# Kernel optimization log

Hardware: AMD Instinct MI355X
Metric: run time of the kernel (lower is better)

The kernel has to match this reference:

```python
import jax, jax.numpy as jnp
import numpy as np

T, B, E, H = 2048, 2, 1024, 16
D = E // H
MAX_REL = 16  # RelativePosition default max_relative_position


def setup_inputs() -> dict:
    key = jax.random.key(0)
    ks = jax.random.split(key, 11)
    s = 1.0 / np.sqrt(E)
    inp = {
        'query': jax.random.normal(ks[0], (T, B, E), dtype=jnp.float32),
        'Wq': jax.random.normal(ks[1], (E, E), dtype=jnp.float32) * s,
        'bq': jnp.zeros((E,), dtype=jnp.float32),
        'Wk': jax.random.normal(ks[2], (E, E), dtype=jnp.float32) * s,
        'bk': jnp.zeros((E,), dtype=jnp.float32),
        'Wv': jax.random.normal(ks[3], (E, E), dtype=jnp.float32) * s,
        'bv': jnp.zeros((E,), dtype=jnp.float32),
        'Wo': jax.random.normal(ks[4], (E, E), dtype=jnp.float32) * s,
        'bo': jnp.zeros((E,), dtype=jnp.float32),
        'rk_table': jax.random.normal(ks[5], (2 * MAX_REL + 1, D), dtype=jnp.float32) * 0.05,
        'rv_table': jax.random.normal(ks[6], (2 * MAX_REL + 1, D), dtype=jnp.float32) * 0.05,
    }
    return inp


def _rel_idx(lq, lk):
    # distance_mat = k - q, clipped to [-MAX_REL, MAX_REL], shifted to [0, 2*MAX_REL]
    d = jnp.arange(lk)[None, :] - jnp.arange(lq)[:, None]
    return jnp.clip(d, -MAX_REL, MAX_REL) + MAX_REL  # [lq, lk] int


def reference(query, Wq, bq, Wk, bk, Wv, bv, Wo, bo, rk_table, rv_table):
    t, b, e = query.shape
    scale = D ** -0.5
    # projections (torch Linear: x @ W.T + b)
    q = (query @ Wq.T + bq) * scale
    k = query @ Wk.T + bk
    v = query @ Wv.T + bv
    # [T,B,E] -> [B*H, T, D]
    q = q.reshape(t, b * H, D).transpose(1, 0, 2)
    k = k.reshape(t, b * H, D).transpose(1, 0, 2)
    v = v.reshape(t, b * H, D).transpose(1, 0, 2)
    # content scores + Shaw relative-position key scores
    scores = jnp.einsum('ntd,nsd->nts', q, k)            # [N, T, S]
    rk = rk_table[_rel_idx(t, t)]                        # [T, S, D]
    scores = scores + jnp.einsum('ntd,tsd->nts', q, rk)  # relpos_k term
    probs = jax.nn.softmax(scores, axis=-1)
    # weighted values + Shaw relative-position value term
    rv = rv_table[_rel_idx(t, t)]                        # [T, S, D]
    attn = jnp.einsum('nts,nsd->ntd', probs, v) + jnp.einsum('nts,tsd->ntd', probs, rv)
    # [B*H, T, D] -> [T, B, E]
    attn = attn.transpose(1, 0, 2).reshape(t, b, e)
    return attn @ Wo.T + bo
```

## Files before the change

kernel.cpp:

```cpp
#include <hip/hip_runtime.h>
#include <hip/hip_bf16.h>
#include <math.h>

#define T_   2048
#define B_   2
#define E_   1024
#define H_   16
#define D_   64
#define NH_  32
#define M_   4096

typedef __attribute__((ext_vector_type(8))) short s8b;
typedef __attribute__((ext_vector_type(4))) float f4;

#define MFMA_B16(a,b,c) __builtin_amdgcn_mfma_f32_16x16x32_bf16(a,b,c,0,0,0)
#define LOG2E 1.44269504088896f

__device__ __forceinline__ unsigned short f2bu(float f) {
    union { __hip_bfloat16 h; unsigned short u; } cv;
    cv.h = __float2bfloat16(f);
    return cv.u;
}
__device__ __forceinline__ unsigned short f2bu_fast(float f) {
    return (unsigned short)((__float_as_uint(f) + 0x8000u) >> 16);
}
__device__ __forceinline__ float bu2f(unsigned short u) {
    union { __hip_bfloat16 h; unsigned short u; } cv; cv.u = u;
    return __bfloat162float(cv.h);
}
__device__ __forceinline__ unsigned int pk2(float a, float b) {
    return (unsigned int)f2bu(a) | ((unsigned int)f2bu(b) << 16);
}
__device__ __forceinline__ unsigned int pk2_fast(float a, float b) {
    return ((__float_as_uint(a) + 0x8000u) >> 16) |
           ((__float_as_uint(b) + 0x8000u) & 0xFFFF0000u);
}
__device__ __forceinline__ float fexp2(float x) {
    return __builtin_amdgcn_exp2f(x);
}
__device__ __forceinline__ float ld1d(const void* p, size_t idx, bool f32) {
    return f32 ? ((const float*)p)[idx] : bu2f(((const unsigned short*)p)[idx]);
}
__device__ __forceinline__ float qsumq(float v) {
    v += __shfl_xor(v, 16); v += __shfl_xor(v, 32);
    return v;
}
__device__ __forceinline__ void glds16(const unsigned short* g, unsigned short* l) {
    __builtin_amdgcn_global_load_lds(
        (const __attribute__((address_space(1))) unsigned int*)g,
        (__attribute__((address_space(3))) unsigned int*)l, 16, 0, 0);
}
__device__ __forceinline__ bool detect_f32(const unsigned short* q16) {
    int e = (q16[threadIdx.x & 63] >> 7) & 0xFF;
    bool sane = (e == 0) || (e >= 97 && e <= 157);
    unsigned long long m = __ballot(sane);
    return __popcll(m) < 56;
}

__global__ __launch_bounds__(256) void cvt_bf16(
    const void* __restrict__ x,
    const void* __restrict__ Wq, const void* __restrict__ Wk,
    const void* __restrict__ Wv, const void* __restrict__ Wo,
    const void* __restrict__ bq, const void* __restrict__ bk,
    const void* __restrict__ bv, const void* __restrict__ bo,
    unsigned short* __restrict__ xw, unsigned short* __restrict__ Ww,
    unsigned short* __restrict__ bw, int* __restrict__ flag)
{
    const bool f32m = detect_f32((const unsigned short*)x);
    const int bid = blockIdx.x;
    if (bid == 0 && threadIdx.x == 0)
        *flag = f32m ? 1 : 0;
    int y, lb;
    if (bid < 2048)       { y = 0;                      lb = bid; }
    else if (bid < 4096)  { y = 1 + ((bid - 2048) >> 9); lb = (bid - 2048) & 511; }
    else                  { y = 5 + (bid - 4096);        lb = 0; }
    const void* src; unsigned short* dst; int n;
    if (y == 0)      { src = x; dst = xw; n = M_ * E_; }
    else if (y <= 4) {
        src = (y == 1) ? Wq : (y == 2) ? Wk : (y == 3) ? Wv : Wo;
        dst = Ww + (size_t)(y - 1) * E_ * E_; n = E_ * E_;
    } else {
        src = (y == 5) ? bq : (y == 6) ? bk : (y == 7) ? bv : bo;
        dst = bw + (size_t)(y - 5) * E_; n = E_;
    }
    int i = (lb * 256 + threadIdx.x) * 8;
    if (i >= n) return;
    if (f32m) {
        const float* s = (const float*)src + i;
        float4 f0 = *(const float4*)s, f1 = *(const float4*)(s + 4);
        union { unsigned int d[4]; s8b v; } u;
        u.d[0] = pk2(f0.x, f0.y); u.d[1] = pk2(f0.z, f0.w);
        u.d[2] = pk2(f1.x, f1.y); u.d[3] = pk2(f1.z, f1.w);
        *(s8b*)(dst + i) = u.v;
    } else {
        *(s8b*)(dst + i) = *(const s8b*)((const unsigned short*)src + i);
    }
}

__global__ __launch_bounds__(256, 3) void qkv_gemm(
    const unsigned short* __restrict__ xw, const unsigned short* __restrict__ Ww,
    const unsigned short* __restrict__ bw,
    unsigned short* __restrict__ qo, unsigned short* __restrict__ ko,
    unsigned short* __restrict__ vo)
{
    const int bid = blockIdx.x;
    const int r_ = bid & 7, s_ = bid >> 3;
    const int g = r_ + 8 * (s_ >> 3);
    const int e0 = (s_ & 7) * 128;
    const int m0 = (g & 31) * 128;
    const int p  = g >> 5;
    const unsigned short* W    = Ww + (size_t)p * E_ * E_;
    const unsigned short* bias = bw + (size_t)p * E_;
    const float scale = (p == 0) ? 0.125f * LOG2E : 1.0f;

    const int tid = threadIdx.x, w = tid >> 6, lane = tid & 63;
    const int quad = lane >> 4, lc = lane & 15;
    const int wx = w & 1, wy = w >> 1;

    __shared__ unsigned short smem[4][128 * 32];

    f4 acc[4][4];
    #pragma unroll
    for (int i = 0; i < 4; i++)
        #pragma unroll
        for (int j = 0; j < 4; j++) acc[i][j] = (f4){0.f, 0.f, 0.f, 0.f};

    const int gr = lane >> 2;
    const int gc = (lane & 3) ^ ((lane >> 2) & 3);
    const size_t aoff = (size_t)(m0 + w*32 + gr) * E_ + gc*8;
    const size_t boff = (size_t)(e0 + w*32 + gr) * E_ + gc*8;

    #pragma unroll
    for (int j = 0; j < 2; j++) {
        glds16(xw + aoff + (size_t)j*16*E_, &smem[0][(w*128 + j*64) * 8]);
        glds16(W  + boff + (size_t)j*16*E_, &smem[2][(w*128 + j*64) * 8]);
    }
    __syncthreads();

    const int fcA = quad ^ (lc & 3);
    for (int k0 = 0; k0 < E_; k0 += 32) {
        const int cur = (k0 >> 5) & 1;
        if (k0 + 32 < E_) {
            #pragma unroll
            for (int j = 0; j < 2; j++) {
                glds16(xw + aoff + (size_t)j*16*E_ + k0 + 32, &smem[cur^1][(w*128 + j*64) * 8]);
                glds16(W  + boff + (size_t)j*16*E_ + k0 + 32, &smem[2 + (cur^1)][(w*128 + j*64) * 8]);
            }
        }
        s8b af[4], bfr[4];
        #pragma unroll
        for (int i = 0; i < 4; i++)
            af[i]  = *(const s8b*)&smem[cur][((wy*64 + i*16 + lc)*4 + fcA) * 8];
        #pragma unroll
        for (int i = 0; i < 4; i++)
            bfr[i] = *(const s8b*)&smem[2 + cur][((wx*64 + i*16 + lc)*4 + fcA) * 8];
        #pragma unroll
        for (int ms = 0; ms < 4; ms++)
            #pragma unroll
            for (int ns = 0; ns < 4; ns++)
                acc[ms][ns] = MFMA_B16(af[ms], bfr[ns], acc[ms][ns]);
        __syncthreads();
    }

    float bias_v[4];
    #pragma unroll
    for (int ns = 0; ns < 4; ns++) bias_v[ns] = bu2f(bias[e0 + wx*64 + ns*16 + lc]);

    unsigned int* cst = (unsigned int*)&smem[0][0];
    if (p < 2) {
        #pragma unroll
        for (int ms = 0; ms < 4; ms++)
            #pragma unroll
            for (int ns = 0; ns < 4; ns++)
                #pragma unroll
                for (int r2 = 0; r2 < 4; r2++) {
                    float val = (acc[ms][ns][r2] + bias_v[ns]) * scale;
                    float nb = __shfl_xor(val, 1);
                    if (!(lane & 1)) {
                        int mi = wy*64 + ms*16 + quad*4 + r2;
                        int ei = wx*64 + ns*16 + lc;
                        int row = ((mi & 1) * 2 + (ei >> 6)) * 64 + (mi >> 1);
                        int col = (ei & 63) >> 1;
                        cst[row*32 + (col ^ ((row & 7) << 2))] = pk2(val, nb);
                    }
                }
        __syncthreads();
        unsigned int* dst32 = (unsigned int*)((p == 0) ? qo : ko);
        #pragma unroll
        for (int i = 0; i < 8; i++) {
            const int li  = i*256 + tid;
            const int row = li >> 3;
            const int ch  = li & 7;
            uint4 vd = *(const uint4*)&cst[row*32 + ((ch*4) ^ ((row & 7) << 2))];
            const int bb = row >> 7, hh = (row >> 6) & 1, tq = row & 63;
            const size_t du = (((size_t)(bb*H_ + (e0 >> 6) + hh) * T_
                                + (m0 >> 1) + tq) << 5) + ch*4;
            *(uint4*)&dst32[du] = vd;
        }
    } else {
        #pragma unroll
        for (int ms = 0; ms < 4; ms++) {
            const int tq = wy*16 + ms*4 + quad;
            #pragma unroll
            for (int ns = 0; ns < 4; ns++) {
                const int e_l = wx*64 + ns*16 + lc;
                const int x = (e_l & 7) << 2;
                float v0 = acc[ms][ns][0] + bias_v[ns];
                float v1 = acc[ms][ns][1] + bias_v[ns];
                float v2 = acc[ms][ns][2] + bias_v[ns];
                float v3 = acc[ms][ns][3] + bias_v[ns];
                cst[e_l*64 + ( tq       ^ x)] = pk2(v0, v2);
                cst[e_l*64 + ((32 + tq) ^ x)] = pk2(v1, v3);
            }
        }
        __syncthreads();
        #pragma unroll
        for (int i = 0; i < 8; i++) {
            const int li  = i*256 + tid;
            const int e_l = li >> 4;
            const int bb  = (li >> 3) & 1;
            const int ch  = li & 7;
            const int x   = (e_l & 7) << 2;
            uint4 vd = *(const uint4*)&cst[e_l*64 + ((bb*32 + ch*4) ^ x)];
            const int e = e0 + e_l, h = e >> 6, d = e & 63;
            const size_t du = ((size_t)(bb*H_ + h) * 64 + d) * (T_/2)
                              + (m0 >> 2) + ch*4;
            *(uint4*)((unsigned int*)vo + du) = vd;
        }
    }
}

__global__ __launch_bounds__(512, 4) void attn_mfma(
    const unsigned short* __restrict__ q, const unsigned short* __restrict__ k,
    const unsigned short* __restrict__ v,
    const void* __restrict__ rk_t, const void* __restrict__ rv_t,
    unsigned short* __restrict__ aout, const int* __restrict__ flag)
{
    const bool f32m = (*flag != 0);
    const int bid = blockIdx.x;
    const int n = bid & 31, qt = bid >> 5;
    const int t0 = qt * 128;
    const int tid = threadIdx.x, w = tid >> 6, lane = tid & 63;
    const int quad = lane >> 4, lc = lane & 15;

    __shared__ unsigned short k_s[2][64 * 64];
    __shared__ unsigned short v_s[2][64 * 64];
    __shared__ unsigned short p_s[8][16 * 72];
    __shared__ unsigned short qrk_s[128 * 36];
    __shared__ unsigned short diag16[128 * 33];
    __shared__ float st_L[128], st_R[128];

    const unsigned short* qn = q + ((size_t)n * T_ + t0) * D_;
    const unsigned short* kn = k + (size_t)n * T_ * D_;
    const unsigned short* vn = v + (size_t)n * D_ * T_;

    s8b qa[2];
    #pragma unroll
    for (int kf = 0; kf < 2; kf++)
        qa[kf] = *(const s8b*)(qn + (size_t)(w*16 + lc) * D_ + kf*32 + quad*8);

    for (int i = tid; i < 128 * 33; i += 512) diag16[i] = 0;

    unsigned int* rks = (unsigned int*)&p_s[0][0];
    for (int i = tid; i < 48 * 36; i += 512) {
        int r = i / 36, c2 = i % 36;
        unsigned int val = 0;
        if (r < 33 && c2 < 32)
            val = pk2(ld1d(rk_t, r*64 + 2*c2, f32m), ld1d(rk_t, r*64 + 2*c2 + 1, f32m));
        rks[i] = val;
    }
    __syncthreads();

    for (int nt = 0; nt < 3; nt++) {
        s8b b0 = *(const s8b*)((const unsigned short*)rks + (nt*16 + lc)*72 + quad*8);
        s8b b1 = *(const s8b*)((const unsigned short*)rks + (nt*16 + lc)*72 + 32 + quad*8);
        f4 a = (f4){0.f, 0.f, 0.f, 0.f};
        a = MFMA_B16(qa[0], b0, a);
        a = MFMA_B16(qa[1], b1, a);
        #pragma unroll
        for (int r = 0; r < 4; r++) {
            float nb = __shfl_xor(a[r], 1);
            int col = nt*16 + lc;
            if (!(lane & 1) && col < 34)
                ((unsigned int*)qrk_s)[(w*16 + quad*4 + r)*18 + (col >> 1)] = pk2(a[r], nb);
        }
    }
    __syncthreads();

    const int t_l = w*16 + lc;
    const float qLn = bu2f(qrk_s[t_l*36 + 0]);
    const float qRn = bu2f(qrk_s[t_l*36 + 32]);
    float L_p = 0.f, R_p = 0.f;
    f4 O[4], lsN, lsL, lsR;
    lsN = (f4){0.f, 0.f, 0.f, 0.f};
    lsL = (f4){0.f, 0.f, 0.f, 0.f};
    lsR = (f4){0.f, 0.f, 0.f, 0.f};
    #pragma unroll
    for (int dt = 0; dt < 4; dt++) O[dt] = (f4){0.f, 0.f, 0.f, 0.f};
    const short ob = (short)0x3F80;
    const s8b ones = { ob, ob, ob, ob, ob, ob, ob, ob };

    const int grr = lane >> 3;
    const int gcc = (lane & 7) ^ grr;
    const size_t koff = (size_t)(w*8 + grr) * D_ + gcc*8;
    const size_t voff = (size_t)(w*8 + grr) * T_ + gcc*8;

    const int kts = ((bid >> 8) & 1) * 16;

    s8b kr0 = *(const s8b*)(kn + koff + (size_t)(kts * 64) * D_);
    s8b vr0 = *(const s8b*)(vn + voff + kts * 64);
    *(s8b*)&k_s[0][(w*64 + lane) * 8] = kr0;
    *(s8b*)&v_s[0][(w*64 + lane) * 8] = vr0;
    __syncthreads();

    const int lc7 = lc & 7;
    for (int it = 0; it < 32; it++) {
        const int kt = (it + kts) & 31;
        const int s0 = kt * 64;
        const int cur = it & 1;
        if (it + 1 < 32) {
            const int s0n = ((it + 1 + kts) & 31) * 64;
            kr0 = *(const s8b*)(kn + koff + (size_t)s0n * D_);
            vr0 = *(const s8b*)(vn + voff + s0n);
        }

        const bool farL  = (s0 + 63 < t0 - 16);
        const bool farR  = (s0 > t0 + 143);
        const bool nearT = !farL && !farR;

        s8b ak[4][2];
        #pragma unroll
        for (int st = 0; st < 4; st++) {
            int row = st*16 + lc;
            ak[st][0] = *(const s8b*)&k_s[cur][(row*8 + (quad       ^ lc7)) * 8];
            ak[st][1] = *(const s8b*)&k_s[cur][(row*8 + ((4 + quad) ^ lc7)) * 8];
        }

        #pragma unroll
        for (int st = 0; st < 4; st++) {
            f4 a;
            if (nearT) a = (f4){0.f, 0.f, 0.f, 0.f};
            else {
                float qb = farL ? qLn : qRn;
                a = (f4){qb, qb, qb, qb};
            }
            a = MFMA_B16(ak[st][0], qa[0], a);
            a = MFMA_B16(ak[st][1], qa[1], a);
            unsigned int lo, hi;
            if (nearT) {
                const int sb = s0 + st*16 + quad*4 - (t0 + t_l);
                unsigned short eb[4];
                #pragma unroll
                for (int r = 0; r < 4; r++) {
                    int rel = sb + r;
                    int rc = rel < -16 ? -16 : (rel > 16 ? 16 : rel);
                    float e = fexp2(a[r] + bu2f(qrk_s[t_l*36 + rc + 16]));
                    eb[r] = f2bu_fast(e);
                    if (rel <= -16)      L_p += e;
                    else if (rel >= 16)  R_p += e;
                    else                 diag16[t_l*33 + rel + 15] = eb[r];
                }
                lo = (unsigned int)eb[0] | ((unsigned int)eb[1] << 16);
                hi = (unsigned int)eb[2] | ((unsigned int)eb[3] << 16);
            } else {
                lo = pk2_fast(fexp2(a[0]), fexp2(a[1]));
                hi = pk2_fast(fexp2(a[2]), fexp2(a[3]));
            }
            *(uint2*)&p_s[w][lc*72 + st*16 + quad*4] = make_uint2(lo, hi);
        }

        s8b pb[2];
        pb[0] = *(const s8b*)&p_s[w][lc*72 + quad*8];
        pb[1] = *(const s8b*)&p_s[w][lc*72 + 32 + quad*8];
        if (nearT) {
            lsN = MFMA_B16(ones, pb[0], lsN);
            lsN = MFMA_B16(ones, pb[1], lsN);
        } else if (farL) {
            lsL = MFMA_B16(ones, pb[0], lsL);
            lsL = MFMA_B16(ones, pb[1], lsL);
        } else {
            lsR = MFMA_B16(ones, pb[0], lsR);
            lsR = MFMA_B16(ones, pb[1], lsR);
        }
        #pragma unroll
        for (int dt = 0; dt < 4; dt++) {
            int row = dt*16 + lc;
            s8b a0 = *(const s8b*)&v_s[cur][(row*8 + (quad       ^ lc7)) * 8];
            s8b a1 = *(const s8b*)&v_s[cur][(row*8 + ((4 + quad) ^ lc7)) * 8];
            O[dt] = MFMA_B16(a0, pb[0], O[dt]);
            O[dt] = MFMA_B16(a1, pb[1], O[dt]);
        }

        if (it + 1 < 32) {
            *(s8b*)&k_s[cur ^ 1][(w*64 + lane) * 8] = kr0;
            *(s8b*)&v_s[cur ^ 1][(w*64 + lane) * 8] = vr0;
        }
        __syncthreads();
    }

    float l = lsN[0] + lsL[0] + lsR[0];
    float L = lsL[0] + qsumq(L_p);
    float R = lsR[0] + qsumq(R_p);
    const float linv = 1.f / l;
    if (quad == 0) { st_L[t_l] = L; st_R[t_l] = R; }
    {
        unsigned int* rvs = (unsigned int*)&k_s[0][0];
        for (int i = tid; i < 64 * 32; i += 512) {
            int d = i >> 5, dwL = i & 31;
            int r0 = dwL * 2, r1 = r0 + 1;
            float x0 = (r0 < 33) ? ld1d(rv_t, (size_t)r0 * 64 + d, f32m) : 0.f;
            float x1 = (r1 < 33) ? ld1d(rv_t, (size_t)r1 * 64 + d, f32m) : 0.f;
            int phys = d * 32 + ((dwL >> 2) ^ (d & 7)) * 4 + (dwL & 3);
            rvs[phys] = pk2(x0, x1);
        }
    }
    __syncthreads();
    for (int j = 0; j < 16; j++) {
        int c = lane;
        int row = w*16 + j;
        unsigned short pv;
        if (c == 0)        pv = f2bu(st_L[row]);
        else if (c == 32)  pv = f2bu(st_R[row]);
        else if (c < 32)   pv = diag16[row*33 + c - 1];
        else               pv = 0;
        p_s[w][j*72 + c] = pv;
    }
    s8b pe[2];
    pe[0] = *(const s8b*)&p_s[w][lc*72 + quad*8];
    pe[1] = *(const s8b*)&p_s[w][lc*72 + 32 + quad*8];
    #pragma unroll
    for (int dt = 0; dt < 4; dt++) {
        int row = dt*16 + lc;
        s8b a0 = *(const s8b*)&k_s[0][(row*8 + (quad       ^ lc7)) * 8];
        s8b a1 = *(const s8b*)&k_s[0][(row*8 + ((4 + quad) ^ lc7)) * 8];
        O[dt] = MFMA_B16(a0, pe[0], O[dt]);
        O[dt] = MFMA_B16(a1, pe[1], O[dt]);
    }
    const int bb = n >> 4, h = n & 15;
    {
        int t_g = t0 + t_l;
        #pragma unroll
        for (int dt = 0; dt < 4; dt++) {
            float v0 = O[dt][0] * linv;
            float v1 = O[dt][1] * linv;
            float v2 = O[dt][2] * linv;
            float v3 = O[dt][3] * linv;
            int e = h*64 + dt*16 + quad*4;
            *(uint2*)&aout[((size_t)t_g * B_ + bb) * E_ + e] =
                make_uint2(pk2(v0, v1), pk2(v2, v3));
        }
    }
}

__global__ __launch_bounds__(256, 2) void out_gemm(
    const unsigned short* __restrict__ A,
    const unsigned short* __restrict__ Wob, const unsigned short* __restrict__ bob,
    void* __restrict__ out, const int* __restrict__ flag)
{
    const bool f32m = (*flag != 0);
    const int bid = blockIdx.x;
    const int r_ = bid & 7, s_ = bid >> 3;
    const int g = r_ + 8 * (s_ >> 3);
    const int m0 = g * 64;
    const int e0 = (s_ & 7) * 128;

    const int tid = threadIdx.x, w = tid >> 6, lane = tid & 63;
    const int quad = lane >> 4, lc = lane & 15;
    const int wx = w & 1, wy = w >> 1;

    __shared__ unsigned short smem[12288];
    #define A_S(c) (&smem[(c) * 2048])
    #define B_S(c) (&smem[4096 + (c) * 4096])

    f4 acc[2][4];
    #pragma unroll
    for (int i = 0; i < 2; i++)
        #pragma unroll
        for (int j = 0; j < 4; j++) acc[i][j] = (f4){0.f, 0.f, 0.f, 0.f};

    const int gr = lane >> 2;
    const int gc = (lane & 3) ^ (gr & 3);
    const size_t aoff = (size_t)(m0 + w*16 + gr) * E_ + gc*8;
    const size_t boff = (size_t)(e0 + w*32 + gr) * E_ + gc*8;

    glds16(A + aoff, &A_S(0)[(w*64) * 8]);
    #pragma unroll
    for (int j = 0; j < 2; j++)
        glds16(Wob + boff + (size_t)j*16*E_, &B_S(0)[(w*128 + j*64) * 8]);
    __syncthreads();

    const int fcA = quad ^ (lc & 3);
    for (int k0 = 0; k0 < E_; k0 += 32) {
        const int cur = (k0 >> 5) & 1;
        if (k0 + 32 < E_) {
            glds16(A + aoff + k0 + 32, &A_S(cur^1)[(w*64) * 8]);
            #pragma unroll
            for (int j = 0; j < 2; j++)
                glds16(Wob + boff + (size_t)j*16*E_ + k0 + 32, &B_S(cur^1)[(w*128 + j*64) * 8]);
        }
        s8b af[2], bfr[4];
        #pragma unroll
        for (int i = 0; i < 2; i++)
            af[i]  = *(const s8b*)&A_S(cur)[((wy*32 + i*16 + lc)*4 + fcA) * 8];
        #pragma unroll
        for (int i = 0; i < 4; i++)
            bfr[i] = *(const s8b*)&B_S(cur)[((wx*64 + i*16 + lc)*4 + fcA) * 8];
        #pragma unroll
        for (int ms = 0; ms < 2; ms++)
            #pragma unroll
            for (int ns = 0; ns < 4; ns++)
                acc[ms][ns] = MFMA_B16(af[ms], bfr[ns], acc[ms][ns]);
        __syncthreads();
    }

    float bias_v[4];
    #pragma unroll
    for (int ns = 0; ns < 4; ns++) bias_v[ns] = bu2f(bob[e0 + wx*64 + ns*16 + lc]);

    if (f32m) {
        #pragma unroll
        for (int ms = 0; ms < 2; ms++)
            #pragma unroll
            for (int ns = 0; ns < 4; ns++)
                #pragma unroll
                for (int r2 = 0; r2 < 4; r2++) {
                    float val = acc[ms][ns][r2] + bias_v[ns];
                    size_t m = m0 + wy*32 + ms*16 + quad*4 + r2;
                    int e = e0 + wx*64 + ns*16 + lc;
                    ((float*)out)[m * E_ + e] = val;
                }
    } else {
        unsigned int* cst = (unsigned int*)&smem[0];
        __syncthreads();
        #pragma unroll
        for (int ms = 0; ms < 2; ms++)
            #pragma unroll
            for (int ns = 0; ns < 4; ns++)
                #pragma unroll
                for (int r2 = 0; r2 < 4; r2++) {
                    float val = acc[ms][ns][r2] + bias_v[ns];
                    float nb = __shfl_xor(val, 1);
                    if (!(lane & 1)) {
                        int mi = wy*32 + ms*16 + quad*4 + r2;
                        int ei = wx*64 + ns*16 + lc;
                        int col = ei >> 1;
                        cst[mi*64 + (col ^ ((mi & 7) << 2))] = pk2(val, nb);
                    }
                }
        __syncthreads();
        unsigned int* dst32 = (unsigned int*)out;
        #pragma unroll
        for (int i = 0; i < 4; i++) {
            const int li  = i*256 + tid;
            const int row = li >> 4;
            const int ch  = li & 15;
            uint4 vd = *(const uint4*)&cst[row*64 + ((ch*4) ^ ((row & 7) << 2))];
            const size_t du = ((size_t)(m0 + row) * E_ + e0) / 2 + ch*4;
            *(uint4*)&dst32[du] = vd;
        }
    }
    #undef A_S
    #undef B_S
}

extern "C" void kernel_launch(void* const* d_in, const int* in_sizes, int n_in,
                              void* d_out, int out_size, void* d_ws, size_t ws_size,
                              hipStream_t stream) {
    const void* x  = d_in[0];
    const void* Wq = d_in[1];  const void* bq = d_in[2];
    const void* Wk = d_in[3];  const void* bk = d_in[4];
    const void* Wv = d_in[5];  const void* bv = d_in[6];
    const void* Wo = d_in[7];  const void* bo = d_in[8];
    const void* rk = d_in[9];  const void* rv = d_in[10];

    int* flag = (int*)d_ws;
    const size_t HTD = (size_t)NH_ * T_ * D_;
    unsigned short* qw = (unsigned short*)((char*)d_ws + 256);
    unsigned short* kw = qw + HTD;
    unsigned short* vw = kw + HTD;
    unsigned short* aw = vw + HTD;
    unsigned short* xw = aw + (size_t)M_ * E_;
    unsigned short* Ww = xw + (size_t)M_ * E_;
    unsigned short* bw = Ww + (size_t)4 * E_ * E_;

    cvt_bf16<<<dim3(4100), 256, 0, stream>>>(
        x, Wq, Wk, Wv, Wo, bq, bk, bv, bo, xw, Ww, bw, flag);
    qkv_gemm<<<dim3(768), 256, 0, stream>>>(xw, Ww, bw, qw, kw, vw);
    attn_mfma<<<dim3(NH_ * (T_/128)), 512, 0, stream>>>(qw, kw, vw, rk, rv, aw, flag);
    out_gemm<<<dim3(512), 256, 0, stream>>>(aw, Ww + (size_t)3*E_*E_, bw + 3*E_,
                                            d_out, flag);
}
```

Before: 208.1 us.

## Switch attention inner loop to 32x32 MFMA with register-resident P via permlane swap

```diff
diff --git a/kernel.cpp b/kernel.cpp
--- a/kernel.cpp
+++ b/kernel.cpp
@@ -12,8 +12,10 @@
 
 typedef __attribute__((ext_vector_type(8))) short s8b;
 typedef __attribute__((ext_vector_type(4))) float f4;
+typedef __attribute__((ext_vector_type(16))) float f16v;
 
 #define MFMA_B16(a,b,c) __builtin_amdgcn_mfma_f32_16x16x32_bf16(a,b,c,0,0,0)
+#define MFMA32(a,b,c)   __builtin_amdgcn_mfma_f32_32x32x16_bf16(a,b,c,0,0,0)
 #define LOG2E 1.44269504088896f
 
 __device__ __forceinline__ unsigned short f2bu(float f) {
@@ -41,9 +43,9 @@
 __device__ __forceinline__ float ld1d(const void* p, size_t idx, bool f32) {
     return f32 ? ((const float*)p)[idx] : bu2f(((const unsigned short*)p)[idx]);
 }
-__device__ __forceinline__ float qsumq(float v) {
-    v += __shfl_xor(v, 16); v += __shfl_xor(v, 32);
-    return v;
+__device__ __forceinline__ void plswap(unsigned int &a, unsigned int &b) {
+    auto r = __builtin_amdgcn_permlane32_swap(a, b, false, false);
+    a = r[0]; b = r[1];
 }
 __device__ __forceinline__ void glds16(const unsigned short* g, unsigned short* l) {
     __builtin_amdgcn_global_load_lds(
@@ -242,22 +244,20 @@
     const int t0 = qt * 128;
     const int tid = threadIdx.x, w = tid >> 6, lane = tid & 63;
     const int quad = lane >> 4, lc = lane & 15;
+    const int tg = w >> 1, sh = w & 1;
+    const int lh = lane >> 5, tloc = lane & 31;
+    const int t_bl = tg * 32 + tloc;
 
     __shared__ unsigned short k_s[2][64 * 64];
     __shared__ unsigned short v_s[2][64 * 64];
-    __shared__ unsigned short p_s[8][16 * 72];
+    __shared__ unsigned short p_s[4][32 * 72];
     __shared__ unsigned short qrk_s[128 * 36];
     __shared__ unsigned short diag16[128 * 33];
-    __shared__ float st_L[128], st_R[128];
+    __shared__ float st3[2][3][128];
 
     const unsigned short* qn = q + ((size_t)n * T_ + t0) * D_;
     const unsigned short* kn = k + (size_t)n * T_ * D_;
     const unsigned short* vn = v + (size_t)n * D_ * T_;
-
-    s8b qa[2];
-    #pragma unroll
-    for (int kf = 0; kf < 2; kf++)
-        qa[kf] = *(const s8b*)(qn + (size_t)(w*16 + lc) * D_ + kf*32 + quad*8);
 
     for (int i = tid; i < 128 * 33; i += 512) diag16[i] = 0;
 
@@ -271,37 +271,44 @@
     }
     __syncthreads();
 
-    for (int nt = 0; nt < 3; nt++) {
-        s8b b0 = *(const s8b*)((const unsigned short*)rks + (nt*16 + lc)*72 + quad*8);
-        s8b b1 = *(const s8b*)((const unsigned short*)rks + (nt*16 + lc)*72 + 32 + quad*8);
-        f4 a = (f4){0.f, 0.f, 0.f, 0.f};
-        a = MFMA_B16(qa[0], b0, a);
-        a = MFMA_B16(qa[1], b1, a);
-        #pragma unroll
-        for (int r = 0; r < 4; r++) {
-            float nb = __shfl_xor(a[r], 1);
-            int col = nt*16 + lc;
-            if (!(lane & 1) && col < 34)
-                ((unsigned int*)qrk_s)[(w*16 + quad*4 + r)*18 + (col >> 1)] = pk2(a[r], nb);
-        }
-    }
-    __syncthreads();
-
-    const int t_l = w*16 + lc;
-    const float qLn = bu2f(qrk_s[t_l*36 + 0]);
-    const float qRn = bu2f(qrk_s[t_l*36 + 32]);
-    float L_p = 0.f, R_p = 0.f;
-    f4 O[4], lsN, lsL, lsR;
-    lsN = (f4){0.f, 0.f, 0.f, 0.f};
-    lsL = (f4){0.f, 0.f, 0.f, 0.f};
-    lsR = (f4){0.f, 0.f, 0.f, 0.f};
-    #pragma unroll
-    for (int dt = 0; dt < 4; dt++) O[dt] = (f4){0.f, 0.f, 0.f, 0.f};
-    const short ob = (short)0x3F80;
-    const s8b ones = { ob, ob, ob, ob, ob, ob, ob, ob };
+    {
+        s8b qa16[2];
+        #pragma unroll
+        for (int kf = 0; kf < 2; kf++)
+            qa16[kf] = *(const s8b*)(qn + (size_t)(w*16 + lc) * D_ + kf*32 + quad*8);
+        for (int nt = 0; nt < 3; nt++) {
+            s8b b0 = *(const s8b*)((const unsigned short*)rks + (nt*16 + lc)*72 + quad*8);
+            s8b b1 = *(const s8b*)((const unsigned short*)rks + (nt*16 + lc)*72 + 32 + quad*8);
+            f4 a = (f4){0.f, 0.f, 0.f, 0.f};
+            a = MFMA_B16(qa16[0], b0, a);
+            a = MFMA_B16(qa16[1], b1, a);
+            #pragma unroll
+            for (int r = 0; r < 4; r++) {
+                float nb = __shfl_xor(a[r], 1);
+                int col = nt*16 + lc;
+                if (!(lane & 1) && col < 34)
+                    ((unsigned int*)qrk_s)[(w*16 + quad*4 + r)*18 + (col >> 1)] = pk2(a[r], nb);
+            }
+        }
+    }
+    __syncthreads();
+
+    s8b qa32[4];
+    #pragma unroll
+    for (int ks = 0; ks < 4; ks++)
+        qa32[ks] = *(const s8b*)(qn + (size_t)t_bl * D_ + ks*16 + lh*8);
+
+    const float qLn = bu2f(qrk_s[t_bl*36 + 0]);
+    const float qRn = bu2f(qrk_s[t_bl*36 + 32]);
+    float L_p = 0.f, R_p = 0.f, sN = 0.f, sL = 0.f, sR = 0.f;
+    f16v O[2];
+    #pragma unroll
+    for (int dt = 0; dt < 2; dt++)
+        #pragma unroll
+        for (int r = 0; r < 16; r++) O[dt][r] = 0.f;
 
     const int grr = lane >> 3;
-    const int gcc = (lane & 7) ^ grr;
+    const int gcc = (lane & 7) ^ grr ^ (w & 1);
     const size_t koff = (size_t)(w*8 + grr) * D_ + gcc*8;
     const size_t voff = (size_t)(w*8 + grr) * T_ + gcc*8;
 
@@ -313,7 +320,8 @@
     *(s8b*)&v_s[0][(w*64 + lane) * 8] = vr0;
     __syncthreads();
 
-    const int lc7 = lc & 7;
+    const int rK   = sh*32 + tloc;
+    const int swzK = (rK & 7) ^ ((rK >> 3) & 1);
     for (int it = 0; it < 32; it++) {
         const int kt = (it + kts) & 31;
         const int s0 = kt * 64;
@@ -328,67 +336,63 @@
         const bool farR  = (s0 > t0 + 143);
         const bool nearT = !farL && !farR;
 
-        s8b ak[4][2];
-        #pragma unroll
-        for (int st = 0; st < 4; st++) {
-            int row = st*16 + lc;
-            ak[st][0] = *(const s8b*)&k_s[cur][(row*8 + (quad       ^ lc7)) * 8];
-            ak[st][1] = *(const s8b*)&k_s[cur][(row*8 + ((4 + quad) ^ lc7)) * 8];
-        }
-
-        #pragma unroll
-        for (int st = 0; st < 4; st++) {
-            f4 a;
-            if (nearT) a = (f4){0.f, 0.f, 0.f, 0.f};
-            else {
-                float qb = farL ? qLn : qRn;
-                a = (f4){qb, qb, qb, qb};
-            }
-            a = MFMA_B16(ak[st][0], qa[0], a);
-            a = MFMA_B16(ak[st][1], qa[1], a);
-            unsigned int lo, hi;
-            if (nearT) {
-                const int sb = s0 + st*16 + quad*4 - (t0 + t_l);
-                unsigned short eb[4];
-                #pragma unroll
-                for (int r = 0; r < 4; r++) {
-                    int rel = sb + r;
-                    int rc = rel < -16 ? -16 : (rel > 16 ? 16 : rel);
-                    float e = fexp2(a[r] + bu2f(qrk_s[t_l*36 + rc + 16]));
-                    eb[r] = f2bu_fast(e);
-                    if (rel <= -16)      L_p += e;
-                    else if (rel >= 16)  R_p += e;
-                    else                 diag16[t_l*33 + rel + 15] = eb[r];
-                }
-                lo = (unsigned int)eb[0] | ((unsigned int)eb[1] << 16);
-                hi = (unsigned int)eb[2] | ((unsigned int)eb[3] << 16);
-            } else {
-                lo = pk2_fast(fexp2(a[0]), fexp2(a[1]));
-                hi = pk2_fast(fexp2(a[2]), fexp2(a[3]));
-            }
-            *(uint2*)&p_s[w][lc*72 + st*16 + quad*4] = make_uint2(lo, hi);
-        }
-
-        s8b pb[2];
-        pb[0] = *(const s8b*)&p_s[w][lc*72 + quad*8];
-        pb[1] = *(const s8b*)&p_s[w][lc*72 + 32 + quad*8];
+        s8b ak32[4];
+        #pragma unroll
+        for (int ks = 0; ks < 4; ks++)
+            ak32[ks] = *(const s8b*)&k_s[cur][(rK*8 + ((2*ks + lh) ^ swzK)) * 8];
+
+        f16v S;
+        {
+            float ini = nearT ? 0.f : (farL ? qLn : qRn);
+            #pragma unroll
+            for (int r = 0; r < 16; r++) S[r] = ini;
+        }
+        #pragma unroll
+        for (int ks = 0; ks < 4; ks++)
+            S = MFMA32(ak32[ks], qa32[ks], S);
+
         if (nearT) {
-            lsN = MFMA_B16(ones, pb[0], lsN);
-            lsN = MFMA_B16(ones, pb[1], lsN);
-        } else if (farL) {
-            lsL = MFMA_B16(ones, pb[0], lsL);
-            lsL = MFMA_B16(ones, pb[1], lsL);
+            #pragma unroll
+            for (int r = 0; r < 16; r++) {
+                int Sl  = (r & 3) + 8*(r >> 2) + 4*lh;
+                int rel = s0 + sh*32 + Sl - (t0 + t_bl);
+                int rc  = rel < -16 ? -16 : (rel > 16 ? 16 : rel);
+                float e = fexp2(S[r] + bu2f(qrk_s[t_bl*36 + rc + 16]));
+                S[r] = e;
+                if (rel <= -16)      L_p += e;
+                else if (rel >= 16)  R_p += e;
+                else                 diag16[t_bl*33 + rel + 15] = f2bu_fast(e);
+            }
         } else {
-            lsR = MFMA_B16(ones, pb[0], lsR);
-            lsR = MFMA_B16(ones, pb[1], lsR);
-        }
-        #pragma unroll
-        for (int dt = 0; dt < 4; dt++) {
-            int row = dt*16 + lc;
-            s8b a0 = *(const s8b*)&v_s[cur][(row*8 + (quad       ^ lc7)) * 8];
-            s8b a1 = *(const s8b*)&v_s[cur][(row*8 + ((4 + quad) ^ lc7)) * 8];
-            O[dt] = MFMA_B16(a0, pb[0], O[dt]);
-            O[dt] = MFMA_B16(a1, pb[1], O[dt]);
+            #pragma unroll
+            for (int r = 0; r < 16; r++) S[r] = fexp2(S[r]);
+        }
+        {
+            float ss = ((S[0]+S[1])+(S[2]+S[3])) + ((S[4]+S[5])+(S[6]+S[7]))
+                     + ((S[8]+S[9])+(S[10]+S[11])) + ((S[12]+S[13])+(S[14]+S[15]));
+            if (nearT) sN += ss; else if (farL) sL += ss; else sR += ss;
+        }
+
+        unsigned int wl[8];
+        #pragma unroll
+        for (int g2 = 0; g2 < 4; g2++) {
+            wl[2*g2]   = pk2_fast(S[4*g2],   S[4*g2+1]);
+            wl[2*g2+1] = pk2_fast(S[4*g2+2], S[4*g2+3]);
+        }
+        plswap(wl[0], wl[2]);  plswap(wl[1], wl[3]);
+        plswap(wl[4], wl[6]);  plswap(wl[5], wl[7]);
+        union { unsigned int d[4]; s8b v; } pb0, pb1;
+        pb0.d[0] = wl[0]; pb0.d[1] = wl[1]; pb0.d[2] = wl[2]; pb0.d[3] = wl[3];
+        pb1.d[0] = wl[4]; pb1.d[1] = wl[5]; pb1.d[2] = wl[6]; pb1.d[3] = wl[7];
+
+        #pragma unroll
+        for (int dt = 0; dt < 2; dt++) {
+            const int rV   = dt*32 + tloc;
+            const int swzV = (rV & 7) ^ ((rV >> 3) & 1);
+            s8b av0 = *(const s8b*)&v_s[cur][(rV*8 + ((sh*4 + 0 + lh) ^ swzV)) * 8];
+            s8b av1 = *(const s8b*)&v_s[cur][(rV*8 + ((sh*4 + 2 + lh) ^ swzV)) * 8];
+            O[dt] = MFMA32(av0, pb0.v, O[dt]);
+            O[dt] = MFMA32(av1, pb1.v, O[dt]);
         }
 
         if (it + 1 < 32) {
@@ -398,11 +402,40 @@
         __syncthreads();
     }
 
-    float l = lsN[0] + lsL[0] + lsR[0];
-    float L = lsL[0] + qsumq(L_p);
-    float R = lsR[0] + qsumq(R_p);
-    const float linv = 1.f / l;
-    if (quad == 0) { st_L[t_l] = L; st_R[t_l] = R; }
+    sN += __shfl_xor(sN, 32);  sL += __shfl_xor(sL, 32);  sR += __shfl_xor(sR, 32);
+    L_p += __shfl_xor(L_p, 32);  R_p += __shfl_xor(R_p, 32);
+    if (lh == 0) {
+        st3[sh][0][t_bl] = sN + sL + sR;
+        st3[sh][1][t_bl] = sL + L_p;
+        st3[sh][2][t_bl] = sR + R_p;
+    }
+    __syncthreads();
+
+    float* obuf = (tg == 0) ? (float*)&k_s[0][0] :
+                  (tg == 1) ? (float*)&k_s[1][0] :
+                  (tg == 2) ? (float*)&v_s[0][0] : (float*)&v_s[1][0];
+    const int xort = (tloc & 7) << 2;
+    if (sh == 1) {
+        #pragma unroll
+        for (int dt = 0; dt < 2; dt++)
+            #pragma unroll
+            for (int r = 0; r < 16; r++) {
+                int Sl = (r & 3) + 8*(r >> 2) + 4*lh;
+                obuf[tloc*64 + ((dt*32 + Sl) ^ xort)] = O[dt][r];
+            }
+    }
+    __syncthreads();
+    if (sh == 0) {
+        #pragma unroll
+        for (int dt = 0; dt < 2; dt++)
+            #pragma unroll
+            for (int r = 0; r < 16; r++) {
+                int Sl = (r & 3) + 8*(r >> 2) + 4*lh;
+                O[dt][r] += obuf[tloc*64 + ((dt*32 + Sl) ^ xort)];
+            }
+    }
+    __syncthreads();
+
     {
         unsigned int* rvs = (unsigned int*)&k_s[0][0];
         for (int i = tid; i < 64 * 32; i += 512) {
@@ -410,45 +443,53 @@
             int r0 = dwL * 2, r1 = r0 + 1;
             float x0 = (r0 < 33) ? ld1d(rv_t, (size_t)r0 * 64 + d, f32m) : 0.f;
             float x1 = (r1 < 33) ? ld1d(rv_t, (size_t)r1 * 64 + d, f32m) : 0.f;
-            int phys = d * 32 + ((dwL >> 2) ^ (d & 7)) * 4 + (dwL & 3);
+            int phys = d * 32 + (((dwL >> 2) ^ (d & 7) ^ ((d >> 3) & 1)) * 4) + (dwL & 3);
             rvs[phys] = pk2(x0, x1);
         }
     }
-    __syncthreads();
     for (int j = 0; j < 16; j++) {
+        int rloc = (w & 1) * 16 + j;
+        int trow = (w >> 1) * 32 + rloc;
         int c = lane;
-        int row = w*16 + j;
         unsigned short pv;
-        if (c == 0)        pv = f2bu(st_L[row]);
-        else if (c == 32)  pv = f2bu(st_R[row]);
-        else if (c < 32)   pv = diag16[row*33 + c - 1];
+        if (c == 0)        pv = f2bu(st3[0][1][trow] + st3[1][1][trow]);
+        else if (c == 32)  pv = f2bu(st3[0][2][trow] + st3[1][2][trow]);
+        else if (c < 32)   pv = diag16[trow*33 + c - 1];
         else               pv = 0;
-        p_s[w][j*72 + c] = pv;
-    }
-    s8b pe[2];
-    pe[0] = *(const s8b*)&p_s[w][lc*72 + quad*8];
-    pe[1] = *(const s8b*)&p_s[w][lc*72 + 32 + quad*8];
-    #pragma unroll
-    for (int dt = 0; dt < 4; dt++) {
-        int row = dt*16 + lc;
-        s8b a0 = *(const s8b*)&k_s[0][(row*8 + (quad       ^ lc7)) * 8];
-        s8b a1 = *(const s8b*)&k_s[0][(row*8 + ((4 + quad) ^ lc7)) * 8];
-        O[dt] = MFMA_B16(a0, pe[0], O[dt]);
-        O[dt] = MFMA_B16(a1, pe[1], O[dt]);
-    }
-    const int bb = n >> 4, h = n & 15;
-    {
-        int t_g = t0 + t_l;
-        #pragma unroll
-        for (int dt = 0; dt < 4; dt++) {
-            float v0 = O[dt][0] * linv;
-            float v1 = O[dt][1] * linv;
-            float v2 = O[dt][2] * linv;
-            float v3 = O[dt][3] * linv;
-            int e = h*64 + dt*16 + quad*4;
-            *(uint2*)&aout[((size_t)t_g * B_ + bb) * E_ + e] =
-                make_uint2(pk2(v0, v1), pk2(v2, v3));
-        }
+        p_s[w >> 1][rloc*72 + c] = pv;
+    }
+    __syncthreads();
+
+    if (sh == 0) {
+        s8b pe[4];
+        #pragma unroll
+        for (int ks = 0; ks < 4; ks++)
+            pe[ks] = *(const s8b*)&p_s[tg][tloc*72 + ks*16 + lh*8];
+        #pragma unroll
+        for (int dt = 0; dt < 2; dt++) {
+            const int rD   = dt*32 + tloc;
+            const int swzD = (rD & 7) ^ ((rD >> 3) & 1);
+            #pragma unroll
+            for (int ks = 0; ks < 4; ks++) {
+                s8b ar = *(const s8b*)&k_s[0][(rD*8 + ((2*ks + lh) ^ swzD)) * 8];
+                O[dt] = MFMA32(ar, pe[ks], O[dt]);
+            }
+        }
+        const int bb = n >> 4, hh = n & 15;
+        const float linv = 1.f / (st3[0][0][t_bl] + st3[1][0][t_bl]);
+        const int t_g = t0 + t_bl;
+        #pragma unroll
+        for (int dt = 0; dt < 2; dt++)
+            #pragma unroll
+            for (int g2 = 0; g2 < 4; g2++) {
+                float v0 = O[dt][4*g2]   * linv;
+                float v1 = O[dt][4*g2+1] * linv;
+                float v2 = O[dt][4*g2+2] * linv;
+                float v3 = O[dt][4*g2+3] * linv;
+                int e = hh*64 + dt*32 + 8*g2 + 4*lh;
+                *(uint2*)&aout[((size_t)t_g * B_ + bb) * E_ + e] =
+                    make_uint2(pk2(v0, v1), pk2(v2, v3));
+            }
     }
 }
 
```

Result: no change. 208.6 us (median of 3 runs) (+0.3%).
